# Optimization experiments

Hardware: AMD Instinct MI355X
Metric: run time of the kernel (lower is better)

Reference implementation:

```python
import jax, jax.numpy as jnp
import numpy as np

B, S = 4, 8192
DIM, H = 1024, 8
C = 2 * H           # num_channels
E = DIM // C        # head_dim = 64
BASE, START, STRIDE = 10.0, 0, 1
CHUNK = 64
EPS = 1e-8
TWO_PI = 2.0 * np.pi


def setup_inputs() -> dict:
    key = jax.random.key(0)
    k1, k2, k3, k4, k5 = jax.random.split(key, 5)
    inputs = jax.random.normal(k1, (B, S, DIM), jnp.float32)
    timestamps = jnp.sort(jax.random.randint(k2, (B, S), 0, 8192, jnp.int32), axis=-1)
    next_timestamps = jnp.sort(jax.random.randint(k3, (B, S), 0, 8192, jnp.int32), axis=-1)
    mask = jnp.ones((B, S), dtype=bool)
    # learned parameters
    Wv = jax.random.normal(k4, (DIM, DIM), jnp.float32) / np.sqrt(DIM)  # proj_v.weight
    gamma_param = jnp.zeros((H,), jnp.float32)
    alpha = jax.random.normal(k5, (C,), jnp.float32) * 0.02
    beta = jnp.ones((C,), jnp.float32)
    return {"inputs": inputs, "Wv": Wv, "gamma_param": gamma_param, "alpha": alpha,
            "beta": beta, "timestamps": timestamps, "next_timestamps": next_timestamps,
            "mask": mask}


def chunkwise_recurrent_attention(q, k, v, decay_steps, mask, chunk):
    # q,k: [B,S,C,2]; v: [B,S,C,E]; decay_steps: [B,S,C]; mask: [B,S] bool
    b, s, c, d = q.shape
    e = v.shape[-1]
    m4 = mask[..., None, None].astype(q.dtype)
    q = q * m4
    k = k * m4
    v = v * m4
    decay = jnp.where(mask[..., None], decay_steps, jnp.ones_like(decay_steps))
    n = s // chunk

    def chunks(x):  # [B,S,...] -> [n,B,L,...]
        return x.reshape(b, n, chunk, *x.shape[2:]).swapaxes(0, 1)

    qc, kc, vc = chunks(q), chunks(k), chunks(v)
    dc = chunks(decay)                       # [n,B,L,C]
    mc = mask.reshape(b, n, chunk).swapaxes(0, 1)
    causal = jnp.tril(jnp.ones((chunk, chunk), q.dtype))

    def step(state, xs):
        qch, kch, vch, dch, mch = xs         # [B,L,C,2],[B,L,C,2],[B,L,C,E],[B,L,C],[B,L]
        prefix = jnp.cumprod(jnp.clip(dch, EPS), axis=1)            # [B,L,C]
        prev = jnp.einsum('blcd,bcde->blce', qch * prefix[..., None], state)
        dmat = prefix[:, :, None, :] / jnp.clip(prefix[:, None, :, :], EPS)  # [B,L,M,C]
        scores = jnp.einsum('blcd,bmcd->blmc', qch, kch)            # [B,L,M,C]
        weights = scores * dmat * causal[None, :, :, None]
        intra = jnp.einsum('blmc,bmce->blce', weights, vch)
        out = (prev + intra) * mch[..., None, None].astype(qch.dtype)
        plast = prefix[:, -1]                                       # [B,C]
        sw = plast[:, None, :] / jnp.clip(prefix, EPS)              # [B,L,C]
        new_state = state * plast[:, :, None, None] + \
            jnp.einsum('blcd,blce->bcde', kch * sw[..., None], vch)
        return new_state, out

    state0 = jnp.zeros((b, c, d, e), q.dtype)
    _, outs = jax.lax.scan(step, state0, (qc, kc, vc, dc, mc))
    return outs.swapaxes(0, 1).reshape(b, s, c, e)


def _forward(inputs, Wv, gamma_param, alpha, beta, timestamps, next_timestamps, mask):
    values = (inputs @ Wv.T).reshape(B, S, C, E)
    scales = jnp.arange(START, START + H * STRIDE, STRIDE, dtype=jnp.float32)
    intervals = jnp.power(BASE, scales).astype(jnp.int32).astype(jnp.float32)  # buffer cast to long
    scale_factor = TWO_PI * jnp.power(1.0 / BASE, scales)
    ts = timestamps.astype(jnp.float32)
    nts = next_timestamps.astype(jnp.float32)
    theta_k = jnp.remainder(ts[..., None], intervals) * scale_factor   # [B,S,H]
    theta_q = jnp.remainder(nts[..., None], intervals) * scale_factor
    key_ = jnp.stack((jnp.cos(theta_k), jnp.sin(theta_k)), axis=-1)    # [B,S,H,2]
    key_ = jnp.concatenate([key_, key_], axis=2)                       # [B,S,C,2]
    cos_q, sin_q = jnp.cos(theta_q), jnp.sin(theta_q)
    query = jnp.concatenate([jnp.stack((sin_q, -cos_q), -1),
                             jnp.stack((cos_q, sin_q), -1)], axis=2)   # [B,S,C,2]
    gamma = jax.nn.sigmoid(gamma_param)
    loggamma = jnp.log(jnp.clip(gamma, 1e-6))
    delta = jnp.clip(nts - ts, 0.0)
    q_decay = jnp.exp(loggamma * (delta[..., None] * scale_factor))    # [B,S,H]
    q_decay = jnp.concatenate([q_decay, q_decay], axis=-1)             # [B,S,C]
    query = query * q_decay[..., None]
    step_delta = jnp.concatenate(
        [jnp.zeros((B, 1), jnp.float32), jnp.clip(ts[:, 1:] - ts[:, :-1], 0.0)], axis=1)
    decay_steps = jnp.exp(loggamma * (step_delta[..., None] * scale_factor))
    decay_steps = jnp.concatenate([decay_steps, decay_steps], axis=-1)  # [B,S,C]
    out = chunkwise_recurrent_attention(query, key_, values, decay_steps, mask, CHUNK)
    out = out * alpha[None, None, :, None] + values * beta[None, None, :, None]
    return out.reshape(B, S, DIM)


def reference(inputs, Wv, gamma_param, alpha, beta, timestamps, next_timestamps, mask):
    return _forward(inputs, Wv, gamma_param, alpha, beta, timestamps, next_timestamps, mask)
```

## Files before the change

### kernel.cpp

```cpp
#include <hip/hip_runtime.h>
#include <stdint.h>

#define SS   8192
#define DIMD 1024
#define NCH  128
#define CC   16
#define EPSF 1e-8f

typedef __bf16 bh;
typedef bh    bhx4 __attribute__((ext_vector_type(4)));
typedef bh    bhx8 __attribute__((ext_vector_type(8)));
typedef float fx4  __attribute__((ext_vector_type(4)));
typedef unsigned int u32x2 __attribute__((ext_vector_type(2)));

#define GLOAD_LDS16(g, l) __builtin_amdgcn_global_load_lds(                    \
    (const __attribute__((address_space(1))) uint32_t*)(g),                    \
    (__attribute__((address_space(3))) uint32_t*)(l), 16, 0, 0)

#define LDSA(p) ((uint32_t)(uintptr_t)(const __attribute__((address_space(3))) char*)(const char*)(p))

#define SB() __builtin_amdgcn_sched_barrier(0)
#define PRE_BAR()  do { SB(); __builtin_amdgcn_s_barrier(); SB();              \
                        __builtin_amdgcn_s_setprio(1); } while (0)
#define POST_BAR() do { __builtin_amdgcn_s_setprio(0); SB();                   \
                        __builtin_amdgcn_s_barrier(); SB(); } while (0)

__global__ __launch_bounds__(256) void cvt_k(const float* __restrict__ src,
                                             bh* __restrict__ dst, int n8) {
    int i = blockIdx.x * 256 + threadIdx.x;
    if (i >= n8) return;
    const float4 a = reinterpret_cast<const float4*>(src)[i * 2];
    const float4 b = reinterpret_cast<const float4*>(src)[i * 2 + 1];
    bhx8 o;
    o[0] = (bh)a.x; o[1] = (bh)a.y; o[2] = (bh)a.z; o[3] = (bh)a.w;
    o[4] = (bh)b.x; o[5] = (bh)b.y; o[6] = (bh)b.z; o[7] = (bh)b.w;
    reinterpret_cast<bhx8*>(dst)[i] = o;
}

template <typename VT>
__global__ __launch_bounds__(512, 2) void gemm256(const bh* __restrict__ A,
                                                  const bh* __restrict__ Bw,
                                                  VT* __restrict__ C) {
    __shared__ __align__(16) char ldsraw[131072];
    const int lb = blockIdx.x;
    const int logical = (lb & 7) * 64 + (lb >> 3);
    const int mt = logical >> 2;
    const int nt = logical & 3;
    const int tid = threadIdx.x, lane = tid & 63, w = tid >> 6;
    const int wm = w >> 2, wn = w & 3;

    fx4 acc[8][4];
#pragma unroll
    for (int i = 0; i < 8; ++i)
#pragma unroll
        for (int j = 0; j < 4; ++j)
#pragma unroll
            for (int r = 0; r < 4; ++r) acc[i][j][r] = 0.f;

    const int kgo = ((tid & 3) ^ ((tid >> 3) & 3)) << 3;
    const bh* gA0 = A  + (size_t)(mt * 256 + (tid >> 2)) * DIMD + kgo;
    const bh* gB0 = Bw + (size_t)(nt * 256 + (tid >> 2)) * DIMD + kgo;

#define STAGE_U(kt, obase, g, h)                                               \
    { char* lp = ldsraw + ((((kt) & 1) * 65536) + (obase) + (h) * 16384) + tid * 16; \
      const bh* gp = (g) + (kt) * 64 + (h) * 32;                               \
      GLOAD_LDS16(gp, lp);                                                     \
      GLOAD_LDS16(gp + 131072, lp + 8192); }

    const int rAb = wm * 128 + (lane & 15);
    const int rBb = wn * 64 + (lane & 15);
    const int s_swz = (lane >> 4) ^ (((lane & 15) >> 1) & 3);
    const int offA = rAb * 64 + s_swz * 16;
    const int offB = rBb * 64 + s_swz * 16;

    STAGE_U(0, 0, gA0, 0); STAGE_U(0, 32768, gB0, 0);
    STAGE_U(0, 0, gA0, 1); STAGE_U(0, 32768, gB0, 1);
    STAGE_U(1, 0, gA0, 0); STAGE_U(1, 32768, gB0, 0);
    STAGE_U(1, 0, gA0, 1); STAGE_U(1, 32768, gB0, 1);
    asm volatile("s_waitcnt vmcnt(8)" ::: "memory");
    SB(); __builtin_amdgcn_s_barrier(); SB();

#pragma unroll 2
    for (int t = 0; t < 16; ++t) {
        const int buf = t & 1;
        const char* pA0 = ldsraw + buf * 65536 + offA;
        const char* pB0 = ldsraw + buf * 65536 + 32768 + offB;
        bhx8 fa[4], fb[4];

#pragma unroll
        for (int i = 0; i < 4; ++i) fa[i] = *reinterpret_cast<const bhx8*>(pA0 + i * 1024);
#pragma unroll
        for (int j = 0; j < 4; ++j) fb[j] = *reinterpret_cast<const bhx8*>(pB0 + j * 1024);
        if (t >= 1 && t <= 14) STAGE_U(t + 1, 0, gA0, 1);
        PRE_BAR();
#pragma unroll
        for (int i = 0; i < 4; ++i)
#pragma unroll
            for (int j = 0; j < 4; ++j)
                acc[i][j] = __builtin_amdgcn_mfma_f32_16x16x32_bf16(fa[i], fb[j], acc[i][j], 0, 0, 0);
        POST_BAR();

#pragma unroll
        for (int i = 0; i < 4; ++i) fa[i] = *reinterpret_cast<const bhx8*>(pA0 + (4 + i) * 1024);
        if (t <= 13) STAGE_U(t + 2, 32768, gB0, 0);
        PRE_BAR();
#pragma unroll
        for (int i = 0; i < 4; ++i)
#pragma unroll
            for (int j = 0; j < 4; ++j)
                acc[4 + i][j] = __builtin_amdgcn_mfma_f32_16x16x32_bf16(fa[i], fb[j], acc[4 + i][j], 0, 0, 0);
        POST_BAR();

#pragma unroll
        for (int i = 0; i < 4; ++i) fa[i] = *reinterpret_cast<const bhx8*>(pA0 + 16384 + i * 1024);
#pragma unroll
        for (int j = 0; j < 4; ++j) fb[j] = *reinterpret_cast<const bhx8*>(pB0 + 16384 + j * 1024);
        if (t <= 13) STAGE_U(t + 2, 0, gA0, 0);
        PRE_BAR();
#pragma unroll
        for (int i = 0; i < 4; ++i)
#pragma unroll
            for (int j = 0; j < 4; ++j)
                acc[i][j] = __builtin_amdgcn_mfma_f32_16x16x32_bf16(fa[i], fb[j], acc[i][j], 0, 0, 0);
        POST_BAR();

#pragma unroll
        for (int i = 0; i < 4; ++i) fa[i] = *reinterpret_cast<const bhx8*>(pA0 + 16384 + (4 + i) * 1024);
        if (t <= 13) STAGE_U(t + 2, 32768, gB0, 1);
        PRE_BAR();
#pragma unroll
        for (int i = 0; i < 4; ++i)
#pragma unroll
            for (int j = 0; j < 4; ++j)
                acc[4 + i][j] = __builtin_amdgcn_mfma_f32_16x16x32_bf16(fa[i], fb[j], acc[4 + i][j], 0, 0, 0);
        __builtin_amdgcn_s_setprio(0);
        if (t < 14)       { asm volatile("s_waitcnt vmcnt(6)" ::: "memory"); }
        else if (t == 14) { asm volatile("s_waitcnt vmcnt(0)" ::: "memory"); }
        SB(); __builtin_amdgcn_s_barrier(); SB();
    }
#undef STAGE_U

    const int r0 = (lane >> 4) * 4;
    const int c0 = lane & 15;
#pragma unroll
    for (int mi = 0; mi < 8; ++mi) {
#pragma unroll
        for (int ni = 0; ni < 4; ++ni) {
            const size_t m = (size_t)(mt * 256 + wm * 128 + mi * 16 + r0);
            const int    n = nt * 256 + wn * 64 + ni * 16 + c0;
#pragma unroll
            for (int r = 0; r < 4; ++r) {
                if constexpr (sizeof(VT) == 2)
                    C[(m + r) * DIMD + n] = (bh)acc[mi][ni][r];
                else
                    C[(m + r) * DIMD + n] = acc[mi][ni][r];
            }
        }
    }
}

__global__ __launch_bounds__(256) void gemm_k(const float* __restrict__ Ain,
                                              const float* __restrict__ Win,
                                              float* __restrict__ Cout) {
    __shared__ __align__(16) char ldsraw[20480];
    char* ldsA = ldsraw;
    char* ldsB = ldsraw + 10240;
    const int tid = threadIdx.x;
    const int lane = tid & 63;
    const int w = tid >> 6;
    const int wm = w >> 1, wn = w & 1;
    const int bid = blockIdx.x;
    const int mt = bid >> 3;
    const int nt = bid & 7;
    const size_t Abase = (size_t)mt * 128 * 1024;
    const size_t Bbase = (size_t)nt * 128 * 1024;
    fx4 acc[4][4];
#pragma unroll
    for (int i = 0; i < 4; i++)
#pragma unroll
        for (int j2 = 0; j2 < 4; j2++)
#pragma unroll
            for (int r = 0; r < 4; r++) acc[i][j2][r] = 0.f;
    const int srow0 = tid >> 3;
    const int sc16 = tid & 7;
    for (int kt = 0; kt < 32; ++kt) {
        const int k0 = kt * 32;
#pragma unroll
        for (int jj = 0; jj < 4; jj++) {
            int row = srow0 + jj * 32;
            const float4 va = *reinterpret_cast<const float4*>(Ain + Abase + (size_t)row * 1024 + k0 + sc16 * 4);
            const float4 vb = *reinterpret_cast<const float4*>(Win + Bbase + (size_t)row * 1024 + k0 + sc16 * 4);
            bhx4 ba, bb2;
            ba[0] = (bh)va.x; ba[1] = (bh)va.y; ba[2] = (bh)va.z; ba[3] = (bh)va.w;
            bb2[0] = (bh)vb.x; bb2[1] = (bh)vb.y; bb2[2] = (bh)vb.z; bb2[3] = (bh)vb.w;
            *reinterpret_cast<bhx4*>(ldsA + row * 80 + sc16 * 8) = ba;
            *reinterpret_cast<bhx4*>(ldsB + row * 80 + sc16 * 8) = bb2;
        }
        __syncthreads();
        bhx8 fa[4], fb[4];
        const int kb = (lane >> 4) * 16;
        const int rA = wm * 64 + (lane & 15);
        const int rB = wn * 64 + (lane & 15);
#pragma unroll
        for (int mi = 0; mi < 4; mi++) fa[mi] = *reinterpret_cast<const bhx8*>(ldsA + (rA + mi * 16) * 80 + kb);
#pragma unroll
        for (int ni = 0; ni < 4; ni++) fb[ni] = *reinterpret_cast<const bhx8*>(ldsB + (rB + ni * 16) * 80 + kb);
#pragma unroll
        for (int mi = 0; mi < 4; mi++)
#pragma unroll
            for (int ni = 0; ni < 4; ni++)
                acc[mi][ni] = __builtin_amdgcn_mfma_f32_16x16x32_bf16(fa[mi], fb[ni], acc[mi][ni], 0, 0, 0);
        __syncthreads();
    }
    const int r0 = (lane >> 4) * 4;
    const int cc0 = lane & 15;
#pragma unroll
    for (int mi = 0; mi < 4; mi++) {
#pragma unroll
        for (int ni = 0; ni < 4; ni++) {
            size_t rr = (size_t)(mt * 128 + wm * 64 + mi * 16 + r0);
            int cc = nt * 128 + wn * 64 + ni * 16 + cc0;
#pragma unroll
            for (int r = 0; r < 4; r++) Cout[(rr + r) * 1024 + cc] = acc[mi][ni][r];
        }
    }
}

template <typename VT>
__global__ __launch_bounds__(64) void ka_k(const int* __restrict__ ts,
                                           const float* __restrict__ gammap,
                                           const VT* values,
                                           float* __restrict__ Aws,
                                           float* __restrict__ plastWs) {
    __shared__ float s_k0[64], s_k1[64];
    int bid = blockIdx.x;
    int j = bid & 127;
    int h = (bid >> 7) & 7;
    int b = bid >> 10;
    int l = threadIdx.x;
    int s = j * 64 + l;
    float iv = 1.f; double invb = 1.0;
    for (int i = 0; i < h; i++) { iv *= 10.f; invb *= 0.1; }
    float sf = (float)(6.283185307179586 * invb);
    float gp = gammap[h];
    float gm = 1.f / (1.f + expf(-gp));
    float lg = logf(fmaxf(gm, 1e-6f));
    int its = ts[b * SS + s];
    int itp = (s > 0) ? ts[b * SS + s - 1] : its;
    int dstep = its - itp; if (dstep < 0) dstep = 0;
    float dec = expf(lg * ((float)dstep * sf));
    float p = fmaxf(dec, EPSF);
#pragma unroll
    for (int off = 1; off < 64; off <<= 1) {
        float o = __shfl_up(p, off, 64);
        if (l >= off) p *= o;
    }
    float plast = __shfl(p, 63, 64);
    float swv = plast / fmaxf(p, EPSF);
    float tk = fmodf((float)its, iv) * sf;
    s_k0[l] = cosf(tk) * swv;
    s_k1[l] = sinf(tk) * swv;
    __syncthreads();
    if (l == 0) {
        plastWs[(b * CC + h) * NCH + j] = plast;
        plastWs[(b * CC + h + 8) * NCH + j] = plast;
    }
    int e = l;
#pragma unroll
    for (int cc2 = 0; cc2 < 2; ++cc2) {
        int c = h + cc2 * 8;
        const VT* vb = values + ((size_t)b * SS + (size_t)j * 64) * DIMD + c * 64 + e;
        float a0 = 0.f, a1 = 0.f;
#pragma unroll 8
        for (int m = 0; m < 64; ++m) {
            float vv = (float)vb[(size_t)m * DIMD];
            a0 += s_k0[m] * vv;
            a1 += s_k1[m] * vv;
        }
        float* ab = Aws + ((size_t)(b * CC + c) * NCH + j) * 128;
        ab[e] = a0;
        ab[64 + e] = a1;
    }
}

__global__ __launch_bounds__(128) void kb_k(const float* __restrict__ Aws,
                                            const float* __restrict__ plastWs,
                                            float* __restrict__ Sws) {
    int bc = blockIdx.x;
    int t = threadIdx.x;
    __shared__ float pl[NCH];
    pl[t] = plastWs[bc * NCH + t];
    __syncthreads();
    float st = 0.f;
    const float* ab = Aws + (size_t)bc * NCH * 128 + t;
    float* sb = Sws + (size_t)bc * NCH * 128 + t;
    for (int j = 0; j < NCH; ++j) {
        sb[(size_t)j * 128] = st;
        st = st * pl[j] + ab[(size_t)j * 128];
    }
}

__global__ __launch_bounds__(256, 2) void kc2_k(const int* __restrict__ ts,
                                                const int* __restrict__ nts,
                                                const float* __restrict__ gammap,
                                                const float* __restrict__ alphap,
                                                const float* __restrict__ betap,
                                                const bh* __restrict__ values,
                                                const float* __restrict__ Sws,
                                                float* __restrict__ outp) {
    __shared__ __align__(16) bh vt[8][4096];
    __shared__ float s_b0[4][64], s_b1[4][64];
    __shared__ float s_a0[8][64], s_a1[8][64];
    __shared__ float s_st0[8][64], s_st1[8][64];

    const int bid = blockIdx.x;
    const int g = bid & 1;
    const int j = (bid >> 1) & 127;
    const int b = bid >> 8;
    const int tid = threadIdx.x, lane = tid & 63, w = tid >> 6;
    const int h = g * 4 + w;
    const int s = j * 64 + lane;

    const int its = ts[b * SS + s];
    const int itp = (s > 0) ? ts[b * SS + s - 1] : its;
    const int inx = nts[b * SS + s];
    const float* swp0 = Sws + ((size_t)(b * CC + h) * NCH + j) * 128;
    const float* swp1 = Sws + ((size_t)(b * CC + h + 8) * NCH + j) * 128;
    const float st00 = swp0[lane], st10 = swp0[64 + lane];
    const float st01 = swp1[lane], st11 = swp1[64 + lane];
    const float al0 = alphap[h], al1 = alphap[h + 8];
    const float be0 = betap[h], be1 = betap[h + 8];
    const float gp = gammap[h];

    const bh* gv0 = values + ((size_t)b * SS + (size_t)j * 64 + (lane >> 1)) * DIMD
                    + h * 64 + (lane & 1) * 8;
    const bh* gv1 = gv0 + 512;
    char* lc0 = (char*)&vt[w * 2][0] + lane * 16;
    char* lc1 = (char*)&vt[w * 2 + 1][0] + lane * 16;
#pragma unroll
    for (int mh = 0; mh < 2; ++mh)
#pragma unroll
        for (int pp = 0; pp < 4; ++pp)
            GLOAD_LDS16(gv0 + mh * 32 * DIMD + pp * 16, lc0 + pp * 2048 + mh * 1024);
#pragma unroll
    for (int mh = 0; mh < 2; ++mh)
#pragma unroll
        for (int pp = 0; pp < 4; ++pp)
            GLOAD_LDS16(gv1 + mh * 32 * DIMD + pp * 16, lc1 + pp * 2048 + mh * 1024);

    float iv = 1.f; double invb = 1.0;
    for (int i = 0; i < h; i++) { iv *= 10.f; invb *= 0.1; }
    const float sf = (float)(6.283185307179586 * invb);
    const float gm = 1.f / (1.f + expf(-gp));
    const float lg = logf(fmaxf(gm, 1e-6f));
    int dstep = its - itp; if (dstep < 0) dstep = 0;
    const float dec = expf(lg * ((float)dstep * sf));
    float p = fmaxf(dec, EPSF);
#pragma unroll
    for (int off = 1; off < 64; off <<= 1) {
        float o = __shfl_up(p, off, 64);
        if (lane >= off) p *= o;
    }
    const float ipv = 1.f / fmaxf(p, EPSF);
    const float tk = fmodf((float)its, iv) * sf;
    const float k0 = cosf(tk), k1 = sinf(tk);
    s_b0[w][lane] = k0 * ipv;
    s_b1[w][lane] = k1 * ipv;
    const float tq = fmodf((float)inx, iv) * sf;
    int dq = inx - its; if (dq < 0) dq = 0;
    const float qd = expf(lg * ((float)dq * sf));
    const float sq = sinf(tq), cq = cosf(tq);
    const int r0i = w * 2, r1i = w * 2 + 1;
    s_a0[r0i][lane] = sq * qd * p * al0;  s_a1[r0i][lane] = -cq * qd * p * al0;
    s_a0[r1i][lane] = cq * qd * p * al1;  s_a1[r1i][lane] = sq * qd * p * al1;
    s_st0[r0i][lane] = st00; s_st1[r0i][lane] = st10;
    s_st0[r1i][lane] = st01; s_st1[r1i][lane] = st11;
    asm volatile("s_waitcnt lgkmcnt(0)" ::: "memory");

    fx4 rb0[2][2], rb1[2][2];
#pragma unroll
    for (int ks = 0; ks < 2; ++ks) {
        const int m0 = ks * 32 + (lane >> 4) * 8;
        rb0[ks][0] = *reinterpret_cast<const fx4*>(&s_b0[w][m0]);
        rb0[ks][1] = *reinterpret_cast<const fx4*>(&s_b0[w][m0 + 4]);
        rb1[ks][0] = *reinterpret_cast<const fx4*>(&s_b1[w][m0]);
        rb1[ks][1] = *reinterpret_cast<const fx4*>(&s_b1[w][m0 + 4]);
    }

#pragma unroll
    for (int cc = 0; cc < 2; ++cc) {
        const int reg = w * 2 + cc;
        const int c = h + cc * 8;
        const char* vbase2 = (const char*)&vt[reg][0];

        bhx8 pa[4][2];
#pragma unroll
        for (int mi = 0; mi < 4; ++mi) {
            const int l = mi * 16 + (lane & 15);
            const float a0l = s_a0[reg][l];
            const float a1l = s_a1[reg][l];
#pragma unroll
            for (int ks = 0; ks < 2; ++ks) {
                if (mi * 16 + 16 <= ks * 32) continue;
                const bool full = (mi * 16 >= ks * 32 + 32);
                bhx8 v;
#pragma unroll
                for (int jj = 0; jj < 8; ++jj) {
                    const int m = ks * 32 + (lane >> 4) * 8 + jj;
                    const float b0m = rb0[ks][jj >> 2][jj & 3];
                    const float b1m = rb1[ks][jj >> 2][jj & 3];
                    const float val = a0l * b0m + a1l * b1m;
                    v[jj] = (full || l >= m) ? (bh)val : (bh)0.f;
                }
                pa[mi][ks] = v;
            }
        }

        if (cc == 0) { asm volatile("s_waitcnt vmcnt(8)" ::: "memory"); }
        else         { asm volatile("s_waitcnt vmcnt(0)" ::: "memory"); }

        const uint32_t tb = LDSA(vbase2) + ((lane >> 4) << 8) + ((lane & 15) << 3);
        bhx8 pb[4][2];
#pragma unroll
        for (int ni = 0; ni < 4; ++ni)
#pragma unroll
            for (int ks = 0; ks < 2; ++ks) {
                const uint32_t a2 = tb + ni * 2048 + ks * 1024;
                u32x2 lo, hi;
                asm volatile("ds_read_b64_tr_b16 %0, %2 offset:0\n\t"
                             "ds_read_b64_tr_b16 %1, %2 offset:128"
                             : "=&v"(lo), "=&v"(hi) : "v"(a2));
                union { u32x2 u[2]; bhx8 f; } u_;
                u_.u[0] = lo; u_.u[1] = hi;
                pb[ni][ks] = u_.f;
            }
        asm volatile("s_waitcnt lgkmcnt(0)" ::: "memory");
        SB();

        fx4 acc[4][4];
#pragma unroll
        for (int mi = 0; mi < 4; ++mi)
#pragma unroll
            for (int ni = 0; ni < 4; ++ni)
#pragma unroll
                for (int r = 0; r < 4; ++r) acc[mi][ni][r] = 0.f;
        __builtin_amdgcn_s_setprio(1);
#pragma unroll
        for (int ks = 0; ks < 2; ++ks)
#pragma unroll
            for (int mi = 0; mi < 4; ++mi) {
                if (mi * 16 + 16 <= ks * 32) continue;
#pragma unroll
                for (int ni = 0; ni < 4; ++ni)
                    acc[mi][ni] = __builtin_amdgcn_mfma_f32_16x16x32_bf16(
                        pa[mi][ks], pb[ni][ks], acc[mi][ni], 0, 0, 0);
            }
        __builtin_amdgcn_s_setprio(0);
        SB();

        float st0e[4], st1e[4];
#pragma unroll
        for (int ni = 0; ni < 4; ++ni) {
            st0e[ni] = s_st0[reg][ni * 16 + (lane & 15)];
            st1e[ni] = s_st1[reg][ni * 16 + (lane & 15)];
        }
        const float bev = (cc == 0) ? be0 : be1;
        float* ob = outp + ((size_t)b * SS + (size_t)j * 64) * DIMD + c * 64 + (lane & 15);
#pragma unroll
        for (int mi = 0; mi < 4; ++mi)
#pragma unroll
            for (int r = 0; r < 4; ++r) {
                const int l = mi * 16 + ((lane >> 4) << 2) + r;
                const float a0l = s_a0[reg][l];
                const float a1l = s_a1[reg][l];
#pragma unroll
                for (int ni = 0; ni < 4; ++ni) {
                    const float vv = (float)*reinterpret_cast<const bh*>(
                        vbase2 + ni * 2048 + (mi * 4 + (lane >> 4)) * 128 + r * 32 + ((lane & 15) << 1));
                    const float o = acc[mi][ni][r] + a0l * st0e[ni] + a1l * st1e[ni] + bev * vv;
                    ob[(size_t)l * DIMD + ni * 16] = o;
                }
            }
    }
}

template <typename VT>
__global__ __launch_bounds__(256) void kc_k(const int* __restrict__ ts,
                                            const int* __restrict__ nts,
                                            const float* __restrict__ gammap,
                                            const float* __restrict__ alphap,
                                            const float* __restrict__ betap,
                                            const VT* values,
                                            const float* __restrict__ Sws,
                                            float* outp) {
    __shared__ float vsm[64][64];
    __shared__ float s_p[64], s_ip[64], s_k0[64], s_k1[64], s_q0[64], s_q1[64];
    __shared__ float s_st[128];
    int bid = blockIdx.x;
    int j = bid & 127;
    int c = (bid >> 7) & 15;
    int b = bid >> 11;
    int h = c & 7;
    int tid = threadIdx.x;
    if (tid < 64) {
        int l = tid;
        int s = j * 64 + l;
        float iv = 1.f; double invb = 1.0;
        for (int i = 0; i < h; i++) { iv *= 10.f; invb *= 0.1; }
        float sf = (float)(6.283185307179586 * invb);
        float gp = gammap[h];
        float gm = 1.f / (1.f + expf(-gp));
        float lg = logf(fmaxf(gm, 1e-6f));
        int its = ts[b * SS + s];
        int itp = (s > 0) ? ts[b * SS + s - 1] : its;
        int dstep = its - itp; if (dstep < 0) dstep = 0;
        float dec = expf(lg * ((float)dstep * sf));
        float p = fmaxf(dec, EPSF);
#pragma unroll
        for (int off = 1; off < 64; off <<= 1) {
            float o = __shfl_up(p, off, 64);
            if (l >= off) p *= o;
        }
        s_p[l] = p;
        s_ip[l] = 1.f / fmaxf(p, EPSF);
        float tk = fmodf((float)its, iv) * sf;
        s_k0[l] = cosf(tk);
        s_k1[l] = sinf(tk);
        int inx = nts[b * SS + s];
        float tq = fmodf((float)inx, iv) * sf;
        int dq = inx - its; if (dq < 0) dq = 0;
        float qd = expf(lg * ((float)dq * sf));
        float sq = sinf(tq), cq2 = cosf(tq);
        s_q0[l] = (c < 8) ? sq * qd : cq2 * qd;
        s_q1[l] = (c < 8) ? (-cq2 * qd) : sq * qd;
    }
    const VT* vbase = values + ((size_t)b * SS + (size_t)j * 64) * DIMD + c * 64;
#pragma unroll
    for (int i = 0; i < 2; ++i) {
        int f = tid + i * 256;
        int row = f >> 3;
        int c8 = f & 7;
        if constexpr (sizeof(VT) == 2) {
            bhx8 v8 = *reinterpret_cast<const bhx8*>(vbase + (size_t)row * DIMD + c8 * 8);
#pragma unroll
            for (int r = 0; r < 8; ++r) vsm[row][c8 * 8 + r] = (float)v8[r];
        } else {
            *reinterpret_cast<float4*>(&vsm[row][c8 * 8]) =
                *reinterpret_cast<const float4*>(vbase + (size_t)row * DIMD + c8 * 8);
            *reinterpret_cast<float4*>(&vsm[row][c8 * 8 + 4]) =
                *reinterpret_cast<const float4*>(vbase + (size_t)row * DIMD + c8 * 8 + 4);
        }
    }
    if (tid < 128) {
        s_st[tid] = Sws[((size_t)(b * CC + c) * NCH + j) * 128 + tid];
    }
    __syncthreads();
    int l = tid >> 2, eg = tid & 3;
    float acc[16];
#pragma unroll
    for (int i = 0; i < 16; i++) acc[i] = 0.f;
    float q0 = s_q0[l], q1 = s_q1[l], pl_ = s_p[l];
    for (int m = 0; m <= l; ++m) {
        float wgt = (q0 * s_k0[m] + q1 * s_k1[m]) * (pl_ * s_ip[m]);
        const float* vr = &vsm[m][eg * 16];
#pragma unroll
        for (int i = 0; i < 16; i++) acc[i] += wgt * vr[i];
    }
    float al = alphap[c], be = betap[c];
    float* ob = outp + ((size_t)b * SS + (size_t)j * 64 + l) * DIMD + c * 64 + eg * 16;
    const float* st0 = &s_st[eg * 16];
    const float* st1 = &s_st[64 + eg * 16];
#pragma unroll
    for (int i2 = 0; i2 < 4; i2++) {
        float4 vv = *reinterpret_cast<const float4*>(&vsm[l][eg * 16 + i2 * 4]);
        float4 o4;
        const float* vvp = (const float*)&vv;
        float* o4p = (float*)&o4;
#pragma unroll
        for (int r = 0; r < 4; r++) {
            int i = i2 * 4 + r;
            float prevt = pl_ * (q0 * st0[i] + q1 * st1[i]);
            o4p[r] = (prevt + acc[i]) * al + vvp[r] * be;
        }
        *reinterpret_cast<float4*>(ob + i2 * 4) = o4;
    }
}

extern "C" void kernel_launch(void* const* d_in, const int* in_sizes, int n_in,
                              void* d_out, int out_size, void* d_ws, size_t ws_size,
                              hipStream_t stream) {
    const float* inputs = (const float*)d_in[0];
    const float* Wv     = (const float*)d_in[1];
    const float* gammap = (const float*)d_in[2];
    const float* alphap = (const float*)d_in[3];
    const float* betap  = (const float*)d_in[4];
    const int*   ts     = (const int*)d_in[5];
    const int*   nts    = (const int*)d_in[6];
    float* outp = (float*)d_out;
    char* ws = (char*)d_ws;

    float* Aws     = (float*)ws;
    float* plastWs = (float*)(ws + 4194304);
    float* Sws     = (float*)(ws + 4227072);
    const size_t base   = 8421376;
    const size_t abytes = 67108864;
    const size_t wbytes = 2097152;
    const size_t vbytes = 67108864;

    if (ws_size >= base + abytes + wbytes + vbytes) {
        bh* Abf = (bh*)(ws + base);
        bh* Wbf = (bh*)(ws + base + abytes);
        bh* Vbf = (bh*)(ws + base + abytes + wbytes);
        cvt_k<<<16384, 256, 0, stream>>>(inputs, Abf, 4194304);
        cvt_k<<<512, 256, 0, stream>>>(Wv, Wbf, 131072);
        gemm256<bh><<<512, 512, 0, stream>>>(Abf, Wbf, Vbf);
        ka_k<bh><<<4096, 64, 0, stream>>>(ts, gammap, Vbf, Aws, plastWs);
        kb_k<<<64, 128, 0, stream>>>(Aws, plastWs, Sws);
        kc2_k<<<1024, 256, 0, stream>>>(ts, nts, gammap, alphap, betap, Vbf, Sws, outp);
    } else if (ws_size >= base + abytes + wbytes) {
        bh* Abf = (bh*)(ws + base);
        bh* Wbf = (bh*)(ws + base + abytes);
        cvt_k<<<16384, 256, 0, stream>>>(inputs, Abf, 4194304);
        cvt_k<<<512, 256, 0, stream>>>(Wv, Wbf, 131072);
        gemm256<float><<<512, 512, 0, stream>>>(Abf, Wbf, outp);
        ka_k<float><<<4096, 64, 0, stream>>>(ts, gammap, outp, Aws, plastWs);
        kb_k<<<64, 128, 0, stream>>>(Aws, plastWs, Sws);
        kc_k<float><<<8192, 256, 0, stream>>>(ts, nts, gammap, alphap, betap, outp, Sws, outp);
    } else {
        gemm_k<<<2048, 256, 0, stream>>>(inputs, Wv, outp);
        ka_k<float><<<4096, 64, 0, stream>>>(ts, gammap, outp, Aws, plastWs);
        kb_k<<<64, 128, 0, stream>>>(Aws, plastWs, Sws);
        kc_k<float><<<8192, 256, 0, stream>>>(ts, nts, gammap, alphap, betap, outp, Sws, outp);
    }
}
```

Measured before the change: 180.3 us.

## Fuse fp32-to-bf16 input conversion into GEMM A-tile loading

Drops the separate conversion pass that turned the fp32 inputs into a bf16 copy in workspace. The GEMM now loads fp32 A tiles through registers, converts them to bf16 and writes them to LDS, while B still uses direct global-to-LDS loads. This removes a full write and re-read of the 64MB bf16 activation copy and one kernel launch. In exchange the GEMM reads twice the A bytes, uses more registers, and needs extra lgkmcnt waits, which may weaken the pipelining of the main loop.

Measured after the change: 221.5 us. 1.23x slower.

```diff
diff --git a/kernel.cpp b/kernel.cpp
--- a/kernel.cpp
+++ b/kernel.cpp
@@ -37,10 +37,14 @@
     reinterpret_cast<bhx8*>(dst)[i] = o;
 }
 
+#define CVT8(v, f0, f1)                                                        \
+    { v[0]=(bh)(f0).x; v[1]=(bh)(f0).y; v[2]=(bh)(f0).z; v[3]=(bh)(f0).w;      \
+      v[4]=(bh)(f1).x; v[5]=(bh)(f1).y; v[6]=(bh)(f1).z; v[7]=(bh)(f1).w; }
+
 template <typename VT>
-__global__ __launch_bounds__(512, 2) void gemm256(const bh* __restrict__ A,
-                                                  const bh* __restrict__ Bw,
-                                                  VT* __restrict__ C) {
+__global__ __launch_bounds__(512, 2) void gemm256f(const float* __restrict__ A,
+                                                   const bh* __restrict__ Bw,
+                                                   VT* __restrict__ C) {
     __shared__ __align__(16) char ldsraw[131072];
     const int lb = blockIdx.x;
     const int logical = (lb & 7) * 64 + (lb >> 3);
@@ -57,13 +61,27 @@
 #pragma unroll
             for (int r = 0; r < 4; ++r) acc[i][j][r] = 0.f;
 
-    const int kgo = ((tid & 3) ^ ((tid >> 3) & 3)) << 3;
-    const bh* gA0 = A  + (size_t)(mt * 256 + (tid >> 2)) * DIMD + kgo;
-    const bh* gB0 = Bw + (size_t)(nt * 256 + (tid >> 2)) * DIMD + kgo;
-
-#define STAGE_U(kt, obase, g, h)                                               \
-    { char* lp = ldsraw + ((((kt) & 1) * 65536) + (obase) + (h) * 16384) + tid * 16; \
-      const bh* gp = (g) + (kt) * 64 + (h) * 32;                               \
+    const int kg8 = ((tid & 3) ^ ((tid >> 3) & 3)) * 8;
+    const float* gAf = A + (size_t)(mt * 256 + (tid >> 2)) * DIMD + kg8;
+    const bh*    gB0 = Bw + (size_t)(nt * 256 + (tid >> 2)) * DIMD + kg8;
+
+#define LDA_ISSUE(kt, h, d)                                                    \
+    { const float* gp = gAf + (kt) * 64 + (h) * 32;                            \
+      (d)[0] = *reinterpret_cast<const float4*>(gp);                           \
+      (d)[1] = *reinterpret_cast<const float4*>(gp + 4);                       \
+      (d)[2] = *reinterpret_cast<const float4*>(gp + 128 * DIMD);              \
+      (d)[3] = *reinterpret_cast<const float4*>(gp + 128 * DIMD + 4); }
+
+#define LDA_WRITE(kt, h, d)                                                    \
+    { char* lp = ldsraw + (((kt) & 1) * 65536 + (h) * 16384) + tid * 16;       \
+      bhx8 v0, v1;                                                             \
+      CVT8(v0, (d)[0], (d)[1]); CVT8(v1, (d)[2], (d)[3]);                      \
+      *reinterpret_cast<bhx8*>(lp) = v0;                                       \
+      *reinterpret_cast<bhx8*>(lp + 8192) = v1; }
+
+#define STAGE_B(kt, h)                                                         \
+    { char* lp = ldsraw + (((kt) & 1) * 65536 + 32768 + (h) * 16384) + tid * 16; \
+      const bh* gp = gB0 + (kt) * 64 + (h) * 32;                               \
       GLOAD_LDS16(gp, lp);                                                     \
       GLOAD_LDS16(gp + 131072, lp + 8192); }
 
@@ -73,25 +91,34 @@
     const int offA = rAb * 64 + s_swz * 16;
     const int offB = rBb * 64 + s_swz * 16;
 
-    STAGE_U(0, 0, gA0, 0); STAGE_U(0, 32768, gB0, 0);
-    STAGE_U(0, 0, gA0, 1); STAGE_U(0, 32768, gB0, 1);
-    STAGE_U(1, 0, gA0, 0); STAGE_U(1, 32768, gB0, 0);
-    STAGE_U(1, 0, gA0, 1); STAGE_U(1, 32768, gB0, 1);
-    asm volatile("s_waitcnt vmcnt(8)" ::: "memory");
-    SB(); __builtin_amdgcn_s_barrier(); SB();
+    {
+        float4 p[16];
+        LDA_ISSUE(0, 0, p);      LDA_ISSUE(0, 1, p + 4);
+        LDA_ISSUE(1, 0, p + 8);  LDA_ISSUE(1, 1, p + 12);
+        STAGE_B(0, 0); STAGE_B(0, 1); STAGE_B(1, 0); STAGE_B(1, 1);
+        LDA_WRITE(0, 0, p);      LDA_WRITE(0, 1, p + 4);
+        LDA_WRITE(1, 0, p + 8);  LDA_WRITE(1, 1, p + 12);
+        asm volatile("s_waitcnt vmcnt(4)" ::: "memory");
+        asm volatile("s_waitcnt lgkmcnt(0)" ::: "memory");
+        SB(); __builtin_amdgcn_s_barrier(); SB();
+    }
+
+    float4 ar[8];
 
 #pragma unroll 2
     for (int t = 0; t < 16; ++t) {
         const int buf = t & 1;
         const char* pA0 = ldsraw + buf * 65536 + offA;
         const char* pB0 = ldsraw + buf * 65536 + 32768 + offB;
+        const bool doA = (t >= 1 && t <= 14);
+        const bool doB = (t <= 13);
         bhx8 fa[4], fb[4];
 
 #pragma unroll
         for (int i = 0; i < 4; ++i) fa[i] = *reinterpret_cast<const bhx8*>(pA0 + i * 1024);
 #pragma unroll
         for (int j = 0; j < 4; ++j) fb[j] = *reinterpret_cast<const bhx8*>(pB0 + j * 1024);
-        if (t >= 1 && t <= 14) STAGE_U(t + 1, 0, gA0, 1);
+        if (doA) { LDA_ISSUE(t + 1, 0, ar); LDA_ISSUE(t + 1, 1, ar + 4); }
         PRE_BAR();
 #pragma unroll
         for (int i = 0; i < 4; ++i)
@@ -102,7 +129,7 @@
 
 #pragma unroll
         for (int i = 0; i < 4; ++i) fa[i] = *reinterpret_cast<const bhx8*>(pA0 + (4 + i) * 1024);
-        if (t <= 13) STAGE_U(t + 2, 32768, gB0, 0);
+        if (doB) STAGE_B(t + 2, 0);
         PRE_BAR();
 #pragma unroll
         for (int i = 0; i < 4; ++i)
@@ -115,7 +142,7 @@
         for (int i = 0; i < 4; ++i) fa[i] = *reinterpret_cast<const bhx8*>(pA0 + 16384 + i * 1024);
 #pragma unroll
         for (int j = 0; j < 4; ++j) fb[j] = *reinterpret_cast<const bhx8*>(pB0 + 16384 + j * 1024);
-        if (t <= 13) STAGE_U(t + 2, 0, gA0, 0);
+        if (doA) LDA_WRITE(t + 1, 0, ar);
         PRE_BAR();
 #pragma unroll
         for (int i = 0; i < 4; ++i)
@@ -126,7 +153,8 @@
 
 #pragma unroll
         for (int i = 0; i < 4; ++i) fa[i] = *reinterpret_cast<const bhx8*>(pA0 + 16384 + (4 + i) * 1024);
-        if (t <= 13) STAGE_U(t + 2, 32768, gB0, 1);
+        if (doB) STAGE_B(t + 2, 1);
+        if (doA) LDA_WRITE(t + 1, 1, ar + 4);
         PRE_BAR();
 #pragma unroll
         for (int i = 0; i < 4; ++i)
@@ -134,11 +162,14 @@
             for (int j = 0; j < 4; ++j)
                 acc[4 + i][j] = __builtin_amdgcn_mfma_f32_16x16x32_bf16(fa[i], fb[j], acc[4 + i][j], 0, 0, 0);
         __builtin_amdgcn_s_setprio(0);
-        if (t < 14)       { asm volatile("s_waitcnt vmcnt(6)" ::: "memory"); }
+        if (t < 14)       { asm volatile("s_waitcnt vmcnt(4)" ::: "memory"); }
         else if (t == 14) { asm volatile("s_waitcnt vmcnt(0)" ::: "memory"); }
+        asm volatile("s_waitcnt lgkmcnt(0)" ::: "memory");
         SB(); __builtin_amdgcn_s_barrier(); SB();
     }
-#undef STAGE_U
+#undef LDA_ISSUE
+#undef LDA_WRITE
+#undef STAGE_B
 
     const int r0 = (lane >> 4) * 4;
     const int c0 = lane & 15;
@@ -603,26 +634,21 @@
     float* plastWs = (float*)(ws + 4194304);
     float* Sws     = (float*)(ws + 4227072);
     const size_t base   = 8421376;
-    const size_t abytes = 67108864;
     const size_t wbytes = 2097152;
     const size_t vbytes = 67108864;
 
-    if (ws_size >= base + abytes + wbytes + vbytes) {
-        bh* Abf = (bh*)(ws + base);
-        bh* Wbf = (bh*)(ws + base + abytes);
-        bh* Vbf = (bh*)(ws + base + abytes + wbytes);
-        cvt_k<<<16384, 256, 0, stream>>>(inputs, Abf, 4194304);
+    if (ws_size >= base + wbytes + vbytes) {
+        bh* Wbf = (bh*)(ws + base);
+        bh* Vbf = (bh*)(ws + base + wbytes);
         cvt_k<<<512, 256, 0, stream>>>(Wv, Wbf, 131072);
-        gemm256<bh><<<512, 512, 0, stream>>>(Abf, Wbf, Vbf);
+        gemm256f<bh><<<512, 512, 0, stream>>>(inputs, Wbf, Vbf);
         ka_k<bh><<<4096, 64, 0, stream>>>(ts, gammap, Vbf, Aws, plastWs);
         kb_k<<<64, 128, 0, stream>>>(Aws, plastWs, Sws);
         kc2_k<<<1024, 256, 0, stream>>>(ts, nts, gammap, alphap, betap, Vbf, Sws, outp);
-    } else if (ws_size >= base + abytes + wbytes) {
-        bh* Abf = (bh*)(ws + base);
-        bh* Wbf = (bh*)(ws + base + abytes);
-        cvt_k<<<16384, 256, 0, stream>>>(inputs, Abf, 4194304);
+    } else if (ws_size >= base + wbytes) {
+        bh* Wbf = (bh*)(ws + base);
         cvt_k<<<512, 256, 0, stream>>>(Wv, Wbf, 131072);
-        gemm256<float><<<512, 512, 0, stream>>>(Abf, Wbf, outp);
+        gemm256f<float><<<512, 512, 0, stream>>>(inputs, Wbf, outp);
         ka_k<float><<<4096, 64, 0, stream>>>(ts, gammap, outp, Aws, plastWs);
         kb_k<<<64, 128, 0, stream>>>(Aws, plastWs, Sws);
         kc_k<float><<<8192, 256, 0, stream>>>(ts, nts, gammap, alphap, betap, outp, Sws, outp);
```

## Fuse per-chunk key-value state reduction into GEMM epilogue

Applied to the files above, without the earlier changes.

Removes the separate ka_k launch by computing the per-chunk decayed key-weighted value sums (Aws) and chunk decay products (plastWs) directly from the GEMM accumulators in registers. This avoids re-reading the projected values from global memory and saves one kernel launch. In exchange the GEMM epilogue gets heavier: it adds transcendental math, warp shuffles and LDS staging, which may raise register pressure in a 512-thread, two-blocks-per-CU kernel. It also reduces fp32 accumulators rather than bf16-rounded values, so numerics differ slightly.

New measurement: 175.1 us. -2.9%, faster.

```diff
diff --git a/kernel.cpp b/kernel.cpp
--- a/kernel.cpp
+++ b/kernel.cpp
@@ -38,9 +38,13 @@
 }
 
 template <typename VT>
-__global__ __launch_bounds__(512, 2) void gemm256(const bh* __restrict__ A,
-                                                  const bh* __restrict__ Bw,
-                                                  VT* __restrict__ C) {
+__global__ __launch_bounds__(512, 2) void gemm256a(const bh* __restrict__ A,
+                                                   const bh* __restrict__ Bw,
+                                                   VT* __restrict__ C,
+                                                   const int* __restrict__ tsp,
+                                                   const float* __restrict__ gammap,
+                                                   float* __restrict__ Aws,
+                                                   float* __restrict__ plastWs) {
     __shared__ __align__(16) char ldsraw[131072];
     const int lb = blockIdx.x;
     const int logical = (lb & 7) * 64 + (lb >> 3);
@@ -155,6 +159,73 @@
                 else
                     C[(m + r) * DIMD + n] = acc[mi][ni][r];
             }
+        }
+    }
+
+    float* wlds = (float*)ldsraw + w * 256;
+    const int b_ = mt >> 5;
+    const int j0 = (mt & 31) * 4;
+    const int c_ = nt * 4 + wn;
+    const int h_ = c_ & 7;
+    float iv = 1.f; double invb = 1.0;
+    for (int i = 0; i < h_; i++) { iv *= 10.f; invb *= 0.1; }
+    const float sf = (float)(6.283185307179586 * invb);
+    const float gm = 1.f / (1.f + expf(-gammap[h_]));
+    const float lg = logf(fmaxf(gm, 1e-6f));
+
+#pragma unroll
+    for (int jl = 0; jl < 2; ++jl) {
+        const int jg = j0 + wm * 2 + jl;
+        const int sl = jg * 64 + lane;
+        const int its = tsp[b_ * SS + sl];
+        const int itp = (sl > 0) ? tsp[b_ * SS + sl - 1] : its;
+        int dstep = its - itp; if (dstep < 0) dstep = 0;
+        const float dec = expf(lg * ((float)dstep * sf));
+        float p = fmaxf(dec, EPSF);
+#pragma unroll
+        for (int off = 1; off < 64; off <<= 1) {
+            float o = __shfl_up(p, off, 64);
+            if (lane >= off) p *= o;
+        }
+        const float plast = __shfl(p, 63, 64);
+        const float swv = plast / fmaxf(p, EPSF);
+        const float tk = fmodf((float)its, iv) * sf;
+        wlds[jl * 128 + lane]      = cosf(tk) * swv;
+        wlds[jl * 128 + 64 + lane] = sinf(tk) * swv;
+        if (lane == 0) plastWs[(size_t)(b_ * CC + c_) * NCH + jg] = plast;
+    }
+    asm volatile("s_waitcnt lgkmcnt(0)" ::: "memory");
+
+#pragma unroll
+    for (int jl = 0; jl < 2; ++jl) {
+        const int jg = j0 + wm * 2 + jl;
+        float* ab = Aws + ((size_t)(b_ * CC + c_) * NCH + jg) * 128;
+        float w0v[16], w1v[16];
+#pragma unroll
+        for (int q = 0; q < 4; ++q)
+#pragma unroll
+            for (int r = 0; r < 4; ++r) {
+                const int ml = q * 16 + ((lane >> 4) << 2) + r;
+                w0v[q * 4 + r] = wlds[jl * 128 + ml];
+                w1v[q * 4 + r] = wlds[jl * 128 + 64 + ml];
+            }
+#pragma unroll
+        for (int ni = 0; ni < 4; ++ni) {
+            float pa0 = 0.f, pa1 = 0.f;
+#pragma unroll
+            for (int q = 0; q < 4; ++q)
+#pragma unroll
+                for (int r = 0; r < 4; ++r) {
+                    const float av = acc[jl * 4 + q][ni][r];
+                    pa0 += w0v[q * 4 + r] * av;
+                    pa1 += w1v[q * 4 + r] * av;
+                }
+            pa0 += __shfl_xor(pa0, 16, 64); pa0 += __shfl_xor(pa0, 32, 64);
+            pa1 += __shfl_xor(pa1, 16, 64); pa1 += __shfl_xor(pa1, 32, 64);
+            const int e = ni * 16 + (lane & 15);
+            const int grp = lane >> 4;
+            if (grp == 0)      ab[e] = pa0;
+            else if (grp == 1) ab[64 + e] = pa1;
         }
     }
 }
@@ -613,8 +684,7 @@
         bh* Vbf = (bh*)(ws + base + abytes + wbytes);
         cvt_k<<<16384, 256, 0, stream>>>(inputs, Abf, 4194304);
         cvt_k<<<512, 256, 0, stream>>>(Wv, Wbf, 131072);
-        gemm256<bh><<<512, 512, 0, stream>>>(Abf, Wbf, Vbf);
-        ka_k<bh><<<4096, 64, 0, stream>>>(ts, gammap, Vbf, Aws, plastWs);
+        gemm256a<bh><<<512, 512, 0, stream>>>(Abf, Wbf, Vbf, ts, gammap, Aws, plastWs);
         kb_k<<<64, 128, 0, stream>>>(Aws, plastWs, Sws);
         kc2_k<<<1024, 256, 0, stream>>>(ts, nts, gammap, alphap, betap, Vbf, Sws, outp);
     } else if (ws_size >= base + abytes + wbytes) {
@@ -622,8 +692,7 @@
         bh* Wbf = (bh*)(ws + base + abytes);
         cvt_k<<<16384, 256, 0, stream>>>(inputs, Abf, 4194304);
         cvt_k<<<512, 256, 0, stream>>>(Wv, Wbf, 131072);
-        gemm256<float><<<512, 512, 0, stream>>>(Abf, Wbf, outp);
-        ka_k<float><<<4096, 64, 0, stream>>>(ts, gammap, outp, Aws, plastWs);
+        gemm256a<float><<<512, 512, 0, stream>>>(Abf, Wbf, outp, ts, gammap, Aws, plastWs);
         kb_k<<<64, 128, 0, stream>>>(Aws, plastWs, Sws);
         kc_k<float><<<8192, 256, 0, stream>>>(ts, nts, gammap, alphap, betap, outp, Sws, outp);
     } else {
```
